# Performance work log

Hardware: AMD Instinct MI355X
Metric: run time of the kernel (lower is better)

The kernel has to match this reference:

```python
import jax, jax.numpy as jnp
import numpy as np

PREV_SIZE = 1024
SIZE = 4096
BATCH = 8192


def setup_inputs() -> dict:
    key = jax.random.key(0)
    k1, k2, k3, k4 = jax.random.split(key, 4)
    return {
        "prev_layer_output": jax.random.normal(k1, (PREV_SIZE, BATCH), dtype=jnp.float32),
        "input_A_weights": jax.random.normal(k2, (SIZE, PREV_SIZE), dtype=jnp.float32),
        "input_B_weights": jax.random.normal(k3, (SIZE, PREV_SIZE), dtype=jnp.float32),
        "table_weights": jax.random.normal(k4, (16, SIZE), dtype=jnp.float32),
    }


def reference(prev_layer_output, input_A_weights, input_B_weights, table_weights):
    # Soft input selection via row-softmax over previous neurons.
    pa = jax.nn.softmax(input_A_weights, axis=1)   # (size, prev_size)
    pb = jax.nn.softmax(input_B_weights, axis=1)   # (size, prev_size)
    pt = jax.nn.softmax(table_weights, axis=0)     # (16, size) softmax over gates

    A = pa @ prev_layer_output                     # (size, batch)
    B = pb @ prev_layer_output                     # (size, batch)
    AB = A * B

    p = pt[:, :, None]                             # (16, size, 1) broadcast over batch
    # Fused weighted sum over the 16 soft logic gates (no (16,size,batch) buffer).
    out = (
        p[1] * AB
        + p[2] * (A - AB)
        + p[3] * A
        + p[4] * (B - AB)
        + p[5] * B
        + p[6] * (A + B - 2.0 * AB)
        + p[7] * (A + B - AB)
        + p[8] * (1.0 - (A + B - AB))
        + p[9] * (1.0 - (A + B - 2.0 * AB))
        + p[10] * (1.0 - B)
        + p[11] * (1.0 - B + AB)
        + p[12] * (1.0 - A)
        + p[13] * (1.0 - A + AB)
        + p[14] * (1.0 - AB)
        + p[15]
    )
    return out
```

## Files before the change

kernel.cpp:

```cpp
#include <hip/hip_runtime.h>
#include <hip/hip_bf16.h>

#define K_DIM 1024
#define M_DIM 4096
#define N_DIM 8192
#define BK 64
#define BM 128
#define BN 256
#define NT 16

#define OFF_A 0
#define OFF_B (BM * BK)
#define OFF_P (2 * BM * BK)
#define BUF_ELEMS (2 * BM * BK + BN * BK)

typedef __attribute__((ext_vector_type(8))) __bf16 bf16x8_t;
typedef __attribute__((ext_vector_type(4))) float f32x4;

#define SBAR do { __builtin_amdgcn_sched_barrier(0); \
                  __builtin_amdgcn_s_barrier(); \
                  __builtin_amdgcn_sched_barrier(0); } while (0)
#define LGKM0 do { asm volatile("s_waitcnt lgkmcnt(0)" ::: "memory"); \
                   __builtin_amdgcn_sched_barrier(0); } while (0)
#define VMCNT(n) do { asm volatile("s_waitcnt vmcnt(" #n ")" ::: "memory"); \
                      __builtin_amdgcn_sched_barrier(0); } while (0)
#define SCHED_FENCE __builtin_amdgcn_sched_barrier(0)

__device__ inline unsigned short f2bf(float f) {
    unsigned u = __float_as_uint(f);
    u += 0x7FFF + ((u >> 16) & 1);
    return (unsigned short)(u >> 16);
}

__device__ __forceinline__ void gload_lds16(const void* g, void* l) {
    __builtin_amdgcn_global_load_lds(
        (const __attribute__((address_space(1))) unsigned int*)g,
        (__attribute__((address_space(3))) unsigned int*)l, 16, 0, 0);
}

__global__ void dual_softmax_kernel(const float* __restrict__ wa,
                                    const float* __restrict__ wb,
                                    unsigned short* __restrict__ pa,
                                    unsigned short* __restrict__ pb) {
    const int idx = blockIdx.x;
    const float* w = (idx < M_DIM) ? wa : wb;
    unsigned short* o = (idx < M_DIM) ? pa : pb;
    const int row = idx & (M_DIM - 1);
    const int tid = threadIdx.x;
    const float4 v = reinterpret_cast<const float4*>(w + (size_t)row * K_DIM)[tid];
    float m = fmaxf(fmaxf(v.x, v.y), fmaxf(v.z, v.w));
    #pragma unroll
    for (int off = 32; off >= 1; off >>= 1) m = fmaxf(m, __shfl_xor(m, off));
    __shared__ float redm[4];
    __shared__ float reds[4];
    if ((tid & 63) == 0) redm[tid >> 6] = m;
    __syncthreads();
    m = fmaxf(fmaxf(redm[0], redm[1]), fmaxf(redm[2], redm[3]));
    const float e0 = __expf(v.x - m), e1 = __expf(v.y - m);
    const float e2 = __expf(v.z - m), e3 = __expf(v.w - m);
    float s = e0 + e1 + e2 + e3;
    #pragma unroll
    for (int off = 32; off >= 1; off >>= 1) s += __shfl_xor(s, off);
    if ((tid & 63) == 0) reds[tid >> 6] = s;
    __syncthreads();
    s = reds[0] + reds[1] + reds[2] + reds[3];
    const float inv = 1.0f / s;
    ushort4 r;
    r.x = f2bf(e0 * inv); r.y = f2bf(e1 * inv);
    r.z = f2bf(e2 * inv); r.w = f2bf(e3 * inv);
    reinterpret_cast<ushort4*>(o + (size_t)row * K_DIM)[tid] = r;
}

__global__ void transpose_conv_kernel(const float* __restrict__ src,
                                      unsigned short* __restrict__ dst) {
    __shared__ float t[32][33];
    const int n0 = blockIdx.x * 32;
    const int k0 = blockIdx.y * 32;
    const int tx = threadIdx.x, ty = threadIdx.y;
    #pragma unroll
    for (int i = ty; i < 32; i += 8)
        t[i][tx] = src[(size_t)(k0 + i) * N_DIM + n0 + tx];
    __syncthreads();
    #pragma unroll
    for (int i = ty; i < 32; i += 8)
        dst[(size_t)(n0 + i) * K_DIM + k0 + tx] = f2bf(t[tx][i]);
}

__global__ void coef_kernel(const float* __restrict__ tw,
                            float4* __restrict__ coef) {
    const int r = blockIdx.x * 256 + threadIdx.x;
    float p[16];
    float m = -1e30f;
    #pragma unroll
    for (int k = 0; k < 16; ++k) { p[k] = tw[k * M_DIM + r]; m = fmaxf(m, p[k]); }
    float s = 0.f;
    #pragma unroll
    for (int k = 0; k < 16; ++k) { p[k] = __expf(p[k] - m); s += p[k]; }
    const float inv = 1.f / s;
    #pragma unroll
    for (int k = 0; k < 16; ++k) p[k] *= inv;
    const float cA  = p[2]+p[3]+p[6]+p[7]-p[8]-p[9]-p[12]-p[13];
    const float cB  = p[4]+p[5]+p[6]+p[7]-p[8]-p[9]-p[10]-p[11];
    const float cAB = p[1]-p[2]-p[4]-2.f*p[6]-p[7]+p[8]+2.f*p[9]+p[11]+p[13]-p[14];
    const float c0  = p[8]+p[9]+p[10]+p[11]+p[12]+p[13]+p[14]+p[15];
    coef[r] = make_float4(cA, cB, cAB, c0);
}

__device__ __forceinline__ void load_frags4(const unsigned short* lbase, int row0,
                                            int fk16, bf16x8_t (&f)[4]) {
    #pragma unroll
    for (int i = 0; i < 4; ++i) {
        const int row = row0 + i * 16;
        f[i] = *reinterpret_cast<const bf16x8_t*>(
            (const char*)lbase + row * 128 + ((fk16 ^ (row & 7)) * 16));
    }
}

__device__ __forceinline__ void mfma_block(const bf16x8_t (&a)[4], const bf16x8_t (&p)[4],
                                           f32x4 (&acc)[4][4]) {
    #pragma unroll
    for (int mi = 0; mi < 4; ++mi)
        #pragma unroll
        for (int ni = 0; ni < 4; ++ni)
            acc[mi][ni] = __builtin_amdgcn_mfma_f32_16x16x32_bf16(
                a[mi], p[ni], acc[mi][ni], 0, 0, 0);
}

__global__ __launch_bounds__(512, 2)
void dual_gemm_kernel(const unsigned short* __restrict__ pa,
                      const unsigned short* __restrict__ pb,
                      const unsigned short* __restrict__ pv,
                      const float4* __restrict__ coef,
                      float* __restrict__ out) {
    __shared__ unsigned short lds[2 * BUF_ELEMS];

    const int tid = threadIdx.x;
    const int lane = tid & 63;
    const int w = tid >> 6;
    const int wm = w >> 2, wn = w & 3;

    const int bm = blockIdx.y;
    const int bn = blockIdx.x;

    const int sub_row = lane >> 3;
    const int scol16  = (lane & 7) ^ sub_row;

    const unsigned short* gA = pa + (size_t)(bm * BM) * K_DIM;
    const unsigned short* gB = pb + (size_t)(bm * BM) * K_DIM;
    const unsigned short* gP = pv + (size_t)(bn * BN) * K_DIM;

    const int fr  = lane & 15;
    const int fkb = lane >> 4;
    const int arow0 = wm * 64 + fr;
    const int prow0 = wn * 64 + fr;

    f32x4 accA[4][4], accB[4][4];
    const f32x4 z = {0.f, 0.f, 0.f, 0.f};
    #pragma unroll
    for (int i = 0; i < 4; ++i)
        #pragma unroll
        for (int j = 0; j < 4; ++j) { accA[i][j] = z; accB[i][j] = z; }

    auto stage = [&](const unsigned short* gbase, int lds_elem_off, int chunk, int k) {
        const int r = chunk * 8 + sub_row;
        const char* src = (const char*)(gbase + (size_t)r * K_DIM + k) + scol16 * 16;
        char* dst = (char*)&lds[lds_elem_off] + chunk * 1024;
        gload_lds16(src, dst);
    };

    bf16x8_t af0[4], pf0[4], bf0[4], af1[4], pf1[4], bf1[4];

    stage(gA, OFF_A, 2 * w, 0);     stage(gA, OFF_A, 2 * w + 1, 0);
    stage(gP, OFF_P, 4 * w, 0);     stage(gP, OFF_P, 4 * w + 1, 0);
    stage(gP, OFF_P, 4 * w + 2, 0); stage(gP, OFF_P, 4 * w + 3, 0);
    stage(gB, OFF_B, 2 * w, 0);     stage(gB, OFF_B, 2 * w + 1, 0);
    VMCNT(0);
    SBAR;
    load_frags4(&lds[OFF_A], arow0, fkb, af0);
    load_frags4(&lds[OFF_P], prow0, fkb, pf0);
    SCHED_FENCE;

    for (int t = 0; t < NT - 1; ++t) {
        const int kn = (t + 1) * BK;
        const int co = (t & 1) * BUF_ELEMS;
        const int no = co ^ BUF_ELEMS;

        stage(gA, no + OFF_A, 2 * w, kn); stage(gA, no + OFF_A, 2 * w + 1, kn);
        stage(gP, no + OFF_P, 4 * w, kn); stage(gP, no + OFF_P, 4 * w + 1, kn);
        stage(gP, no + OFF_P, 4 * w + 2, kn); stage(gP, no + OFF_P, 4 * w + 3, kn);
        LGKM0;
        load_frags4(&lds[co + OFF_B], arow0, fkb, bf0);
        SCHED_FENCE;
        __builtin_amdgcn_s_setprio(1);
        mfma_block(af0, pf0, accA);
        __builtin_amdgcn_s_setprio(0);
        SBAR;

        stage(gB, no + OFF_B, 2 * w, kn); stage(gB, no + OFF_B, 2 * w + 1, kn);
        LGKM0;
        load_frags4(&lds[co + OFF_A], arow0, fkb + 4, af1);
        load_frags4(&lds[co + OFF_P], prow0, fkb + 4, pf1);
        SCHED_FENCE;
        __builtin_amdgcn_s_setprio(1);
        mfma_block(bf0, pf0, accB);
        __builtin_amdgcn_s_setprio(0);
        SBAR;

        VMCNT(2);
        LGKM0;
        load_frags4(&lds[co + OFF_B], arow0, fkb + 4, bf1);
        SCHED_FENCE;
        __builtin_amdgcn_s_setprio(1);
        mfma_block(af1, pf1, accA);
        __builtin_amdgcn_s_setprio(0);
        SBAR;

        VMCNT(0);
        LGKM0;
        load_frags4(&lds[no + OFF_A], arow0, fkb, af0);
        load_frags4(&lds[no + OFF_P], prow0, fkb, pf0);
        SCHED_FENCE;
        __builtin_amdgcn_s_setprio(1);
        mfma_block(bf1, pf1, accB);
        __builtin_amdgcn_s_setprio(0);
        SBAR;
    }

    {
        const int co = ((NT - 1) & 1) * BUF_ELEMS;
        LGKM0;
        load_frags4(&lds[co + OFF_B], arow0, fkb, bf0);
        SCHED_FENCE;
        mfma_block(af0, pf0, accA);
        LGKM0;
        load_frags4(&lds[co + OFF_A], arow0, fkb + 4, af1);
        load_frags4(&lds[co + OFF_P], prow0, fkb + 4, pf1);
        SCHED_FENCE;
        mfma_block(bf0, pf0, accB);
        LGKM0;
        load_frags4(&lds[co + OFF_B], arow0, fkb + 4, bf1);
        SCHED_FENCE;
        mfma_block(af1, pf1, accA);
        LGKM0;
        mfma_block(bf1, pf1, accB);
    }

    const int row_grp = lane >> 4;
    #pragma unroll
    for (int mi = 0; mi < 4; ++mi) {
        #pragma unroll
        for (int ni = 0; ni < 4; ++ni) {
            const int gr0 = bm * BM + wm * 64 + mi * 16 + row_grp * 4;
            const int gc  = bn * BN + wn * 64 + ni * 16 + (lane & 15);
            #pragma unroll
            for (int i = 0; i < 4; ++i) {
                const int r = gr0 + i;
                const float4 cf = coef[r];
                const float av = accA[mi][ni][i];
                const float bv = accB[mi][ni][i];
                out[(size_t)r * N_DIM + gc] =
                    fmaf(cf.z, av * bv, fmaf(cf.x, av, fmaf(cf.y, bv, cf.w)));
            }
        }
    }
}

extern "C" void kernel_launch(void* const* d_in, const int* in_sizes, int n_in,
                              void* d_out, int out_size, void* d_ws, size_t ws_size,
                              hipStream_t stream) {
    const float* prev = (const float*)d_in[0];
    const float* wa   = (const float*)d_in[1];
    const float* wb   = (const float*)d_in[2];
    const float* tw   = (const float*)d_in[3];
    float* out = (float*)d_out;

    char* ws = (char*)d_ws;
    unsigned short* pa = (unsigned short*)ws;
    unsigned short* pb = (unsigned short*)(ws + 8388608);
    unsigned short* pv = (unsigned short*)(ws + 16777216);
    float4* coef       = (float4*)(ws + 33554432);

    dual_softmax_kernel<<<2 * M_DIM, 256, 0, stream>>>(wa, wb, pa, pb);
    transpose_conv_kernel<<<dim3(N_DIM / 32, K_DIM / 32), dim3(32, 8), 0, stream>>>(prev, pv);
    coef_kernel<<<M_DIM / 256, 256, 0, stream>>>(tw, coef);
    dual_gemm_kernel<<<dim3(N_DIM / BN, M_DIM / BM), 512, 0, stream>>>(pa, pb, pv, coef, out);
}
```

Measured before the change: 155.1 us.

## Restructure dual-GEMM main loop schedule and drop sched_barrier fences

Reworks the K-loop pipeline so fragment loads from LDS are issued at the start of each phase, not prefetched across phases. Global-to-LDS staging of B now comes first, then A and P. Barriers move from one per phase to two per phase, and a single vmcnt(0) replaces the split vmcnt waits. All sched_barrier fences are removed, handing instruction scheduling back to the compiler. Each phase now exposes its LDS load latency, though the compiler may interleave loads and MFMAs more freely.

```diff
diff --git a/kernel.cpp b/kernel.cpp
--- a/kernel.cpp
+++ b/kernel.cpp
@@ -10,21 +10,16 @@
 #define NT 16
 
 #define OFF_A 0
-#define OFF_B (BM * BK)
-#define OFF_P (2 * BM * BK)
-#define BUF_ELEMS (2 * BM * BK + BN * BK)
+#define OFF_B 16384
+#define OFF_P 32768
+#define BUF_BYTES 65536
 
 typedef __attribute__((ext_vector_type(8))) __bf16 bf16x8_t;
 typedef __attribute__((ext_vector_type(4))) float f32x4;
 
-#define SBAR do { __builtin_amdgcn_sched_barrier(0); \
-                  __builtin_amdgcn_s_barrier(); \
-                  __builtin_amdgcn_sched_barrier(0); } while (0)
-#define LGKM0 do { asm volatile("s_waitcnt lgkmcnt(0)" ::: "memory"); \
-                   __builtin_amdgcn_sched_barrier(0); } while (0)
-#define VMCNT(n) do { asm volatile("s_waitcnt vmcnt(" #n ")" ::: "memory"); \
-                      __builtin_amdgcn_sched_barrier(0); } while (0)
-#define SCHED_FENCE __builtin_amdgcn_sched_barrier(0)
+#define SBAR __builtin_amdgcn_s_barrier()
+#define LGKM0 asm volatile("s_waitcnt lgkmcnt(0)" ::: "memory")
+#define VMCNT0 asm volatile("s_waitcnt vmcnt(0)" ::: "memory")
 
 __device__ inline unsigned short f2bf(float f) {
     unsigned u = __float_as_uint(f);
@@ -118,12 +113,14 @@
 
 __device__ __forceinline__ void mfma_block(const bf16x8_t (&a)[4], const bf16x8_t (&p)[4],
                                            f32x4 (&acc)[4][4]) {
+    __builtin_amdgcn_s_setprio(1);
     #pragma unroll
     for (int mi = 0; mi < 4; ++mi)
         #pragma unroll
         for (int ni = 0; ni < 4; ++ni)
             acc[mi][ni] = __builtin_amdgcn_mfma_f32_16x16x32_bf16(
                 a[mi], p[ni], acc[mi][ni], 0, 0, 0);
+    __builtin_amdgcn_s_setprio(0);
 }
 
 __global__ __launch_bounds__(512, 2)
@@ -132,15 +129,13 @@
                       const unsigned short* __restrict__ pv,
                       const float4* __restrict__ coef,
                       float* __restrict__ out) {
-    __shared__ unsigned short lds[2 * BUF_ELEMS];
+    __shared__ unsigned short lds[2 * BUF_BYTES / 2];
 
     const int tid = threadIdx.x;
     const int lane = tid & 63;
     const int w = tid >> 6;
     const int wm = w >> 2, wn = w & 3;
-
-    const int bm = blockIdx.y;
-    const int bn = blockIdx.x;
+    const int bm = blockIdx.y, bn = blockIdx.x;
 
     const int sub_row = lane >> 3;
     const int scol16  = (lane & 7) ^ sub_row;
@@ -161,87 +156,72 @@
         #pragma unroll
         for (int j = 0; j < 4; ++j) { accA[i][j] = z; accB[i][j] = z; }
 
-    auto stage = [&](const unsigned short* gbase, int lds_elem_off, int chunk, int k) {
+    auto stage = [&](const unsigned short* gbase, int lds_byte_off, int chunk, int k) {
         const int r = chunk * 8 + sub_row;
         const char* src = (const char*)(gbase + (size_t)r * K_DIM + k) + scol16 * 16;
-        char* dst = (char*)&lds[lds_elem_off] + chunk * 1024;
+        char* dst = (char*)lds + lds_byte_off + chunk * 1024;
         gload_lds16(src, dst);
     };
 
-    bf16x8_t af0[4], pf0[4], bf0[4], af1[4], pf1[4], bf1[4];
-
+    stage(gB, OFF_B, 2 * w, 0);     stage(gB, OFF_B, 2 * w + 1, 0);
     stage(gA, OFF_A, 2 * w, 0);     stage(gA, OFF_A, 2 * w + 1, 0);
     stage(gP, OFF_P, 4 * w, 0);     stage(gP, OFF_P, 4 * w + 1, 0);
     stage(gP, OFF_P, 4 * w + 2, 0); stage(gP, OFF_P, 4 * w + 3, 0);
-    stage(gB, OFF_B, 2 * w, 0);     stage(gB, OFF_B, 2 * w + 1, 0);
-    VMCNT(0);
+    VMCNT0;
     SBAR;
-    load_frags4(&lds[OFF_A], arow0, fkb, af0);
-    load_frags4(&lds[OFF_P], prow0, fkb, pf0);
-    SCHED_FENCE;
 
     for (int t = 0; t < NT - 1; ++t) {
         const int kn = (t + 1) * BK;
-        const int co = (t & 1) * BUF_ELEMS;
-        const int no = co ^ BUF_ELEMS;
-
+        const int co = (t & 1) * BUF_BYTES;
+        const int no = co ^ BUF_BYTES;
+        const unsigned short* cb = (const unsigned short*)((const char*)lds + co);
+        bf16x8_t af0[4], pf0[4], bf0[4], af1[4], pf1[4], bf1[4];
+
+        load_frags4((const unsigned short*)((const char*)cb + OFF_A), arow0, fkb, af0);
+        load_frags4((const unsigned short*)((const char*)cb + OFF_P), prow0, fkb, pf0);
+        stage(gB, no + OFF_B, 2 * w, kn); stage(gB, no + OFF_B, 2 * w + 1, kn);
+        SBAR;
+        LGKM0;
+        mfma_block(af0, pf0, accA);
+        SBAR;
+
+        load_frags4((const unsigned short*)((const char*)cb + OFF_B), arow0, fkb, bf0);
         stage(gA, no + OFF_A, 2 * w, kn); stage(gA, no + OFF_A, 2 * w + 1, kn);
         stage(gP, no + OFF_P, 4 * w, kn); stage(gP, no + OFF_P, 4 * w + 1, kn);
         stage(gP, no + OFF_P, 4 * w + 2, kn); stage(gP, no + OFF_P, 4 * w + 3, kn);
-        LGKM0;
-        load_frags4(&lds[co + OFF_B], arow0, fkb, bf0);
-        SCHED_FENCE;
-        __builtin_amdgcn_s_setprio(1);
+        SBAR;
+        LGKM0;
+        mfma_block(bf0, pf0, accB);
+        SBAR;
+
+        load_frags4((const unsigned short*)((const char*)cb + OFF_A), arow0, fkb + 4, af1);
+        load_frags4((const unsigned short*)((const char*)cb + OFF_P), prow0, fkb + 4, pf1);
+        SBAR;
+        LGKM0;
+        mfma_block(af1, pf1, accA);
+        SBAR;
+
+        load_frags4((const unsigned short*)((const char*)cb + OFF_B), arow0, fkb + 4, bf1);
+        VMCNT0;
+        SBAR;
+        LGKM0;
+        mfma_block(bf1, pf1, accB);
+        SBAR;
+    }
+
+    {
+        const unsigned short* cb =
+            (const unsigned short*)((const char*)lds + ((NT - 1) & 1) * BUF_BYTES);
+        bf16x8_t af0[4], pf0[4], bf0[4], af1[4], pf1[4], bf1[4];
+        load_frags4((const unsigned short*)((const char*)cb + OFF_A), arow0, fkb, af0);
+        load_frags4((const unsigned short*)((const char*)cb + OFF_P), prow0, fkb, pf0);
         mfma_block(af0, pf0, accA);
-        __builtin_amdgcn_s_setprio(0);
-        SBAR;
-
-        stage(gB, no + OFF_B, 2 * w, kn); stage(gB, no + OFF_B, 2 * w + 1, kn);
-        LGKM0;
-        load_frags4(&lds[co + OFF_A], arow0, fkb + 4, af1);
-        load_frags4(&lds[co + OFF_P], prow0, fkb + 4, pf1);
-        SCHED_FENCE;
-        __builtin_amdgcn_s_setprio(1);
+        load_frags4((const unsigned short*)((const char*)cb + OFF_B), arow0, fkb, bf0);
         mfma_block(bf0, pf0, accB);
-        __builtin_amdgcn_s_setprio(0);
-        SBAR;
-
-        VMCNT(2);
-        LGKM0;
-        load_frags4(&lds[co + OFF_B], arow0, fkb + 4, bf1);
-        SCHED_FENCE;
-        __builtin_amdgcn_s_setprio(1);
+        load_frags4((const unsigned short*)((const char*)cb + OFF_A), arow0, fkb + 4, af1);
+        load_frags4((const unsigned short*)((const char*)cb + OFF_P), prow0, fkb + 4, pf1);
         mfma_block(af1, pf1, accA);
-        __builtin_amdgcn_s_setprio(0);
-        SBAR;
-
-        VMCNT(0);
-        LGKM0;
-        load_frags4(&lds[no + OFF_A], arow0, fkb, af0);
-        load_frags4(&lds[no + OFF_P], prow0, fkb, pf0);
-        SCHED_FENCE;
-        __builtin_amdgcn_s_setprio(1);
-        mfma_block(bf1, pf1, accB);
-        __builtin_amdgcn_s_setprio(0);
-        SBAR;
-    }
-
-    {
-        const int co = ((NT - 1) & 1) * BUF_ELEMS;
-        LGKM0;
-        load_frags4(&lds[co + OFF_B], arow0, fkb, bf0);
-        SCHED_FENCE;
-        mfma_block(af0, pf0, accA);
-        LGKM0;
-        load_frags4(&lds[co + OFF_A], arow0, fkb + 4, af1);
-        load_frags4(&lds[co + OFF_P], prow0, fkb + 4, pf1);
-        SCHED_FENCE;
-        mfma_block(bf0, pf0, accB);
-        LGKM0;
-        load_frags4(&lds[co + OFF_B], arow0, fkb + 4, bf1);
-        SCHED_FENCE;
-        mfma_block(af1, pf1, accA);
-        LGKM0;
+        load_frags4((const unsigned short*)((const char*)cb + OFF_B), arow0, fkb + 4, bf1);
         mfma_block(bf1, pf1, accB);
     }
 
```

Measured after the change: 155.8 us. No clear change (+0.5%).
